# Optimization experiments

Measured on AMD Instinct MI355X. Metric: run time of the kernel, lower is better.

The kernel has to match this reference:

```python
import jax, jax.numpy as jnp
import numpy as np
import math

# AAMsoftmax constants (m=0.2, s=30), matching the torch implementation
M = 0.2
S = 30.0
COS_M = math.cos(M)
SIN_M = math.sin(M)
TH = math.cos(math.pi - M)
MM = math.sin(math.pi - M) * M

B, IN, P, C = 4096, 1024, 256, 5994


def _l2norm(v):
    # F.normalize: v / max(||v||, eps)
    n = jnp.sqrt(jnp.sum(v * v, axis=-1, keepdims=True))
    return v / jnp.maximum(n, 1e-12)


def setup_inputs() -> dict:
    key = jax.random.key(0)
    k0, k1, k2, k3 = jax.random.split(key, 4)
    return {
        "x": jax.random.normal(k0, (B, IN), jnp.float32),
        "label": jax.random.randint(k1, (B,), 0, C, dtype=jnp.int32),
        "W_fc": jax.random.normal(k2, (P, IN), jnp.float32) * (1.0 / np.sqrt(IN)),
        "b_fc": jnp.zeros((P,), jnp.float32),
        "W_aam": jax.random.normal(k3, (C, P), jnp.float32) * 0.05,
    }


def reference(x, label, W_fc, b_fc, W_aam):
    # fc layer: [B, IN] -> [B, P]
    e = x @ W_fc.T + b_fc
    # cosine similarity against class prototypes: [B, C]
    cosine = _l2norm(e) @ _l2norm(W_aam).T
    sine = jnp.sqrt(jnp.clip(1.0 - cosine * cosine, 0.0, 1.0))
    phi = cosine * COS_M - sine * SIN_M
    # easy-margin-off fallback: use cosine - mm where angle too large
    phi = jnp.where((cosine - TH) > 0, phi, cosine - MM)
    one_hot = jax.nn.one_hot(label, C, dtype=cosine.dtype)
    logits = (one_hot * phi + (1.0 - one_hot) * cosine) * S
    # cross-entropy (mean over batch)
    logp = jax.nn.log_softmax(logits, axis=-1)
    nll = -jnp.take_along_axis(logp, label[:, None].astype(jnp.int32), axis=1)[:, 0]
    return jnp.mean(nll)
```

## Files before the change

kernel.cpp:

```cpp
#include <hip/hip_runtime.h>
#include <math.h>

typedef __attribute__((ext_vector_type(8))) short bf16x8;
typedef __attribute__((ext_vector_type(4))) float f32x4;

#define AAM_COS_M 0.9800665778412416f
#define AAM_SIN_M 0.19866933079506122f
#define AAM_TH   (-0.9800665778412416f)
#define AAM_MM    0.03973386615901225f
#define C_CLS 5994

__device__ inline ushort f2bf(float f) {
    unsigned x = __float_as_uint(f);
    return (ushort)((x + 0x7fffu + ((x >> 16) & 1u)) >> 16);
}
__device__ inline float bflo(unsigned u) { return __uint_as_float(u << 16); }
__device__ inline float bfhi(unsigned u) { return __uint_as_float(u & 0xffff0000u); }

__device__ __forceinline__ void gload16(const void* g, void* lds) {
    __builtin_amdgcn_global_load_lds(
        (const __attribute__((address_space(1))) unsigned int*)g,
        (__attribute__((address_space(3))) unsigned int*)lds, 16, 0, 0);
}

__global__ __launch_bounds__(256) void prep(const float* __restrict__ x,
                                            const float* __restrict__ Wfc,
                                            const float* __restrict__ Waam,
                                            ushort* __restrict__ xb,
                                            ushort* __restrict__ wfcb,
                                            ushort* __restrict__ Wn) {
    const int b = blockIdx.x;
    if (b < 4352) {
        const float* s = (b < 4096) ? x : Wfc;
        ushort* d      = (b < 4096) ? xb : wfcb;
        int i = (b < 4096 ? b : b - 4096) * 256 + threadIdx.x;
        float4 v = ((const float4*)s)[i];
        ushort4 o;
        o.x = f2bf(v.x); o.y = f2bf(v.y); o.z = f2bf(v.z); o.w = f2bf(v.w);
        ((ushort4*)d)[i] = o;
    } else {
        const int wave = threadIdx.x >> 6, lane = threadIdx.x & 63;
        const int row = (b - 4352) * 4 + wave;
        ushort4 o;
        if (row < C_CLS) {
            float4 v = ((const float4*)&Waam[(size_t)row * 256])[lane];
            float ss = v.x * v.x + v.y * v.y + v.z * v.z + v.w * v.w;
#pragma unroll
            for (int m = 32; m >= 1; m >>= 1) ss += __shfl_xor(ss, m, 64);
            float sc = 1.f / fmaxf(sqrtf(ss), 1e-12f);
            o.x = f2bf(v.x * sc); o.y = f2bf(v.y * sc);
            o.z = f2bf(v.z * sc); o.w = f2bf(v.w * sc);
        } else {
            o.x = 0; o.y = 0; o.z = 0; o.w = 0;
        }
        ((ushort4*)&Wn[(size_t)row * 256])[lane] = o;
    }
}

__global__ __launch_bounds__(256) void fc_mfma(const ushort* __restrict__ A,
                                               const ushort* __restrict__ Bm,
                                               const float* __restrict__ bias,
                                               float* __restrict__ C) {
    __shared__ ushort As[64 * 32];
    __shared__ ushort Bs[64 * 32];
    const int tid = threadIdx.x, lane = tid & 63, w = tid >> 6;
    const int wr = w >> 1, wc = w & 1;
    const int lx = lane & 15, lg = lane >> 4;
    const int l4 = lane >> 2, c8 = (lane & 3) << 3;
    const int rb = blockIdx.x * 64, cb = blockIdx.y * 64;

    f32x4 zero = {0.f, 0.f, 0.f, 0.f};
    f32x4 acc[2][2];
#pragma unroll
    for (int i = 0; i < 2; ++i)
#pragma unroll
        for (int j = 0; j < 2; ++j) acc[i][j] = zero;

    for (int k0 = 0; k0 < 1024; k0 += 32) {
        gload16(&A[(size_t)(rb + w * 16 + l4) * 1024 + k0 + c8], &As[w * 512]);
        gload16(&Bm[(size_t)(cb + w * 16 + l4) * 1024 + k0 + c8], &Bs[w * 512]);
        __syncthreads();
        bf16x8 af[2], bv[2];
#pragma unroll
        for (int f = 0; f < 2; ++f) {
            af[f] = *(const bf16x8*)&As[(wr * 32 + f * 16 + lx) * 32 + lg * 8];
            bv[f] = *(const bf16x8*)&Bs[(wc * 32 + f * 16 + lx) * 32 + lg * 8];
        }
#pragma unroll
        for (int i = 0; i < 2; ++i)
#pragma unroll
            for (int j = 0; j < 2; ++j)
                acc[i][j] = __builtin_amdgcn_mfma_f32_16x16x32_bf16(af[i], bv[j], acc[i][j], 0, 0, 0);
        __syncthreads();
    }
#pragma unroll
    for (int j = 0; j < 2; ++j) {
        int col = cb + wc * 32 + j * 16 + lx;
        float bb = bias[col];
#pragma unroll
        for (int i = 0; i < 2; ++i) {
            int row0 = rb + wr * 32 + i * 16 + lg * 4;
#pragma unroll
            for (int r = 0; r < 4; ++r)
                C[(size_t)(row0 + r) * 256 + col] = acc[i][j][r] + bb;
        }
    }
}

__global__ __launch_bounds__(256) void rownorm_e(const float* __restrict__ E,
                                                 ushort* __restrict__ En) {
    const int wave = threadIdx.x >> 6, lane = threadIdx.x & 63;
    const int row = blockIdx.x * 4 + wave;
    float4 v = ((const float4*)&E[(size_t)row * 256])[lane];
    float ss = v.x * v.x + v.y * v.y + v.z * v.z + v.w * v.w;
#pragma unroll
    for (int m = 32; m >= 1; m >>= 1) ss += __shfl_xor(ss, m, 64);
    float sc = 1.f / fmaxf(sqrtf(ss), 1e-12f);
    ushort4 o;
    o.x = f2bf(v.x * sc); o.y = f2bf(v.y * sc); o.z = f2bf(v.z * sc); o.w = f2bf(v.w * sc);
    ((ushort4*)&En[(size_t)row * 256])[lane] = o;
}

__global__ __launch_bounds__(256, 2) void aam_mfma(const ushort* __restrict__ A,
                                                   const ushort* __restrict__ Bm,
                                                   const int* __restrict__ lab,
                                                   float* __restrict__ ps,
                                                   float* __restrict__ cosl) {
    __shared__ ushort As[2][128 * 64];
    __shared__ ushort Bs[2][128 * 64];
    const int tid = threadIdx.x, lane = tid & 63, w = tid >> 6;
    const int wr = w >> 1, wc = w & 1;
    const int lx = lane & 15, lg = lane >> 4;
    const int rb = blockIdx.x * 128;
    const int split = blockIdx.y;

    const int lrow = lane >> 3;
    const int gcol = ((lane & 7) ^ lrow) * 8;

    int labs[16];
#pragma unroll
    for (int idx = 0; idx < 16; ++idx)
        labs[idx] = lab[rb + wr * 64 + (idx >> 2) * 16 + lg * 4 + (idx & 3)];

    float srun[16];
#pragma unroll
    for (int idx = 0; idx < 16; ++idx) srun[idx] = 0.f;

    f32x4 zero = {0.f, 0.f, 0.f, 0.f};
    f32x4 acc[4][4];
#pragma unroll
    for (int i = 0; i < 4; ++i)
#pragma unroll
        for (int j = 0; j < 4; ++j) acc[i][j] = zero;

#define AAM_STAGE(buf, g) do {                                                  \
    int t_ = (g) >> 2, k0_ = ((g) & 3) * 64;                                    \
    int cb_ = split * 384 + t_ * 128;                                           \
    _Pragma("unroll")                                                           \
    for (int s_ = 0; s_ < 4; ++s_) {                                            \
        int r0_ = w * 32 + s_ * 8;                                              \
        gload16(&A[(size_t)(rb + r0_ + lrow) * 256 + k0_ + gcol],               \
                &As[buf][r0_ * 64]);                                            \
        gload16(&Bm[(size_t)(cb_ + r0_ + lrow) * 256 + k0_ + gcol],             \
                &Bs[buf][r0_ * 64]);                                            \
    } } while (0)

    int cur = 0;
    AAM_STAGE(0, 0);
    __syncthreads();

    for (int g = 0; g < 12; ++g) {
        if (g < 11) AAM_STAGE(cur ^ 1, g + 1);
#pragma unroll
        for (int kk = 0; kk < 2; ++kk) {
            bf16x8 af[4], bv[4];
#pragma unroll
            for (int f = 0; f < 4; ++f) {
                int ra = wr * 64 + f * 16 + lx;
                int ca = (lg + kk * 4) ^ (lx & 7);
                af[f] = *(const bf16x8*)&As[cur][ra * 64 + ca * 8];
                int rq = wc * 64 + f * 16 + lx;
                bv[f] = *(const bf16x8*)&Bs[cur][rq * 64 + ca * 8];
            }
#pragma unroll
            for (int i = 0; i < 4; ++i)
#pragma unroll
                for (int j = 0; j < 4; ++j)
                    acc[i][j] = __builtin_amdgcn_mfma_f32_16x16x32_bf16(af[i], bv[j], acc[i][j], 0, 0, 0);
        }
        if ((g & 3) == 3) {
            int cb_ = split * 384 + (g >> 2) * 128;
#pragma unroll
            for (int j = 0; j < 4; ++j) {
                int c = cb_ + wc * 64 + j * 16 + lx;
                if (c < C_CLS) {
#pragma unroll
                    for (int i = 0; i < 4; ++i)
#pragma unroll
                        for (int r = 0; r < 4; ++r) {
                            int idx = i * 4 + r;
                            float cosv = acc[i][j][r];
                            srun[idx] += __expf(30.f * cosv - 30.f);
                            if (c == labs[idx])
                                cosl[rb + wr * 64 + i * 16 + lg * 4 + r] = cosv;
                        }
                }
            }
#pragma unroll
            for (int i = 0; i < 4; ++i)
#pragma unroll
                for (int j = 0; j < 4; ++j) acc[i][j] = zero;
        }
        __syncthreads();
        cur ^= 1;
    }
#undef AAM_STAGE

#pragma unroll
    for (int idx = 0; idx < 16; ++idx) {
#pragma unroll
        for (int msk = 1; msk < 16; msk <<= 1)
            srun[idx] += __shfl_xor(srun[idx], msk, 64);
        if (lx == 0) {
            int row = rb + wr * 64 + (idx >> 2) * 16 + lg * 4 + (idx & 3);
            ps[(size_t)row * 32 + split * 2 + wc] = srun[idx];
        }
    }
}

__global__ __launch_bounds__(256) void reduce_nll(const float* __restrict__ ps,
                                                  const float* __restrict__ cosl,
                                                  float* __restrict__ partial) {
    __shared__ float red[4];
    const int row = blockIdx.x * 256 + threadIdx.x;
    const int wave = threadIdx.x >> 6, lane = threadIdx.x & 63;
    float s = 0.f;
#pragma unroll
    for (int q = 0; q < 8; ++q) {
        float4 v = ((const float4*)&ps[(size_t)row * 32])[q];
        s += v.x + v.y + v.z + v.w;
    }
    float cv = cosl[row];
    float sine = sqrtf(fmaxf(1.f - cv * cv, 0.f));
    float phi = cv * AAM_COS_M - sine * AAM_SIN_M;
    phi = ((cv - AAM_TH) > 0.f) ? phi : (cv - AAM_MM);
    float denom = s - __expf(30.f * cv - 30.f) + __expf(30.f * phi - 30.f);
    float nll = 30.f + logf(denom) - 30.f * phi;
#pragma unroll
    for (int m = 32; m >= 1; m >>= 1) nll += __shfl_xor(nll, m, 64);
    if (lane == 0) red[wave] = nll;
    __syncthreads();
    if (threadIdx.x == 0)
        partial[blockIdx.x] = red[0] + red[1] + red[2] + red[3];
}

__global__ __launch_bounds__(64) void final_reduce(const float* __restrict__ partial,
                                                   float* __restrict__ out) {
    const int lane = threadIdx.x;
    float v = (lane < 16) ? partial[lane] : 0.f;
#pragma unroll
    for (int m = 32; m >= 1; m >>= 1) v += __shfl_xor(v, m, 64);
    if (lane == 0) out[0] = v * (1.f / 4096.f);
}

extern "C" void kernel_launch(void* const* d_in, const int* in_sizes, int n_in,
                              void* d_out, int out_size, void* d_ws, size_t ws_size,
                              hipStream_t stream) {
    const float* x    = (const float*)d_in[0];
    const int*   lab  = (const int*)d_in[1];
    const float* Wfc  = (const float*)d_in[2];
    const float* bfc  = (const float*)d_in[3];
    const float* Waam = (const float*)d_in[4];
    float* out = (float*)d_out;

    char* ws = (char*)d_ws;
    ushort* xb   = (ushort*)(ws);
    ushort* Wfcb = (ushort*)(ws + 8388608);
    float*  E    = (float*) (ws + 8912896);
    ushort* En   = (ushort*)(ws);
    ushort* Wn   = (ushort*)(ws + 13107200);
    float*  ps   = (float*) (ws + 16252928);
    float*  cosl = (float*) (ws + 16777216);
    float*  part = (float*) (ws + 16793600);

    prep<<<5888, 256, 0, stream>>>(x, Wfc, Waam, xb, Wfcb, Wn);
    fc_mfma<<<dim3(64, 4), 256, 0, stream>>>(xb, Wfcb, bfc, E);
    rownorm_e<<<1024, 256, 0, stream>>>(E, En);
    aam_mfma<<<dim3(32, 16), 256, 0, stream>>>(En, Wn, lab, ps, cosl);
    reduce_nll<<<16, 256, 0, stream>>>(ps, cosl, part);
    final_reduce<<<1, 64, 0, stream>>>(part, out);
}
```

Before: 120.3 us.

## Fuse fc GEMM with bias and row L2-normalization, convert x to bf16 in-kernel

The separate x-to-bf16 conversion pass and the fp32 E round-trip plus rownorm kernel are removed. A new fc_norm kernel loads fp32 x tiles straight into LDS and converts them to bf16 in registers. Each block computes a full 16x256 output row tile with double-buffered staging, then adds bias, L2-normalizes across waves through shared memory and writes bf16 En directly. This cuts two launches and roughly 16MB of global traffic, but uses only 256 blocks with small per-block M, which may hurt GEMM efficiency and occupancy.

```diff
diff --git a/kernel.cpp b/kernel.cpp
--- a/kernel.cpp
+++ b/kernel.cpp
@@ -14,8 +14,6 @@
     unsigned x = __float_as_uint(f);
     return (ushort)((x + 0x7fffu + ((x >> 16) & 1u)) >> 16);
 }
-__device__ inline float bflo(unsigned u) { return __uint_as_float(u << 16); }
-__device__ inline float bfhi(unsigned u) { return __uint_as_float(u & 0xffff0000u); }
 
 __device__ __forceinline__ void gload16(const void* g, void* lds) {
     __builtin_amdgcn_global_load_lds(
@@ -23,24 +21,20 @@
         (__attribute__((address_space(3))) unsigned int*)lds, 16, 0, 0);
 }
 
-__global__ __launch_bounds__(256) void prep(const float* __restrict__ x,
-                                            const float* __restrict__ Wfc,
+__global__ __launch_bounds__(256) void prep(const float* __restrict__ Wfc,
                                             const float* __restrict__ Waam,
-                                            ushort* __restrict__ xb,
                                             ushort* __restrict__ wfcb,
                                             ushort* __restrict__ Wn) {
     const int b = blockIdx.x;
-    if (b < 4352) {
-        const float* s = (b < 4096) ? x : Wfc;
-        ushort* d      = (b < 4096) ? xb : wfcb;
-        int i = (b < 4096 ? b : b - 4096) * 256 + threadIdx.x;
-        float4 v = ((const float4*)s)[i];
+    if (b < 256) {
+        int i = b * 256 + threadIdx.x;
+        float4 v = ((const float4*)Wfc)[i];
         ushort4 o;
         o.x = f2bf(v.x); o.y = f2bf(v.y); o.z = f2bf(v.z); o.w = f2bf(v.w);
-        ((ushort4*)d)[i] = o;
+        ((ushort4*)wfcb)[i] = o;
     } else {
         const int wave = threadIdx.x >> 6, lane = threadIdx.x & 63;
-        const int row = (b - 4352) * 4 + wave;
+        const int row = (b - 256) * 4 + wave;
         ushort4 o;
         if (row < C_CLS) {
             float4 v = ((const float4*)&Waam[(size_t)row * 256])[lane];
@@ -57,68 +51,95 @@
     }
 }
 
-__global__ __launch_bounds__(256) void fc_mfma(const ushort* __restrict__ A,
+__global__ __launch_bounds__(256) void fc_norm(const float* __restrict__ X,
                                                const ushort* __restrict__ Bm,
                                                const float* __restrict__ bias,
-                                               float* __restrict__ C) {
-    __shared__ ushort As[64 * 32];
-    __shared__ ushort Bs[64 * 32];
+                                               ushort* __restrict__ En) {
+    __shared__ float  Af[2][16 * 32];
+    __shared__ ushort Bs[2][256 * 32];
+    __shared__ float  red[4][16];
     const int tid = threadIdx.x, lane = tid & 63, w = tid >> 6;
-    const int wr = w >> 1, wc = w & 1;
     const int lx = lane & 15, lg = lane >> 4;
-    const int l4 = lane >> 2, c8 = (lane & 3) << 3;
-    const int rb = blockIdx.x * 64, cb = blockIdx.y * 64;
+    const int rb = blockIdx.x * 16;
+
+    const int arow = lane >> 3;
+    const int agcol = ((lane & 7) ^ arow) * 4;
+    const int brow = lane >> 2;
+    const int bgcol = (((lane & 3) ^ (brow & 3)) * 8);
 
     f32x4 zero = {0.f, 0.f, 0.f, 0.f};
-    f32x4 acc[2][2];
-#pragma unroll
-    for (int i = 0; i < 2; ++i)
-#pragma unroll
-        for (int j = 0; j < 2; ++j) acc[i][j] = zero;
-
-    for (int k0 = 0; k0 < 1024; k0 += 32) {
-        gload16(&A[(size_t)(rb + w * 16 + l4) * 1024 + k0 + c8], &As[w * 512]);
-        gload16(&Bm[(size_t)(cb + w * 16 + l4) * 1024 + k0 + c8], &Bs[w * 512]);
+    f32x4 acc[4];
+#pragma unroll
+    for (int j = 0; j < 4; ++j) acc[j] = zero;
+
+#define FC_STAGE(buf, k0) do {                                                  \
+    if (w < 2)                                                                  \
+        gload16(&X[(size_t)(rb + w * 8 + arow) * 1024 + (k0) + agcol],          \
+                &Af[buf][w * 256]);                                             \
+    _Pragma("unroll")                                                           \
+    for (int s_ = 0; s_ < 4; ++s_) {                                            \
+        int r0_ = w * 64 + s_ * 16;                                             \
+        gload16(&Bm[(size_t)(r0_ + brow) * 1024 + (k0) + bgcol],                \
+                &Bs[buf][r0_ * 32]);                                            \
+    } } while (0)
+
+    int cur = 0;
+    FC_STAGE(0, 0);
+    __syncthreads();
+
+    for (int g = 0; g < 32; ++g) {
+        if (g < 31) FC_STAGE(cur ^ 1, (g + 1) * 32);
+        float4 fa0 = *(const float4*)&Af[cur][lx * 32 + (((lg * 2)     ^ (lx & 7)) * 4)];
+        float4 fa1 = *(const float4*)&Af[cur][lx * 32 + (((lg * 2 + 1) ^ (lx & 7)) * 4)];
+        bf16x8 af;
+        af[0] = (short)f2bf(fa0.x); af[1] = (short)f2bf(fa0.y);
+        af[2] = (short)f2bf(fa0.z); af[3] = (short)f2bf(fa0.w);
+        af[4] = (short)f2bf(fa1.x); af[5] = (short)f2bf(fa1.y);
+        af[6] = (short)f2bf(fa1.z); af[7] = (short)f2bf(fa1.w);
+        bf16x8 bv[4];
+#pragma unroll
+        for (int j = 0; j < 4; ++j) {
+            int rq = w * 64 + j * 16 + lx;
+            bv[j] = *(const bf16x8*)&Bs[cur][rq * 32 + ((lg ^ (rq & 3)) * 8)];
+        }
+#pragma unroll
+        for (int j = 0; j < 4; ++j)
+            acc[j] = __builtin_amdgcn_mfma_f32_16x16x32_bf16(af, bv[j], acc[j], 0, 0, 0);
         __syncthreads();
-        bf16x8 af[2], bv[2];
-#pragma unroll
-        for (int f = 0; f < 2; ++f) {
-            af[f] = *(const bf16x8*)&As[(wr * 32 + f * 16 + lx) * 32 + lg * 8];
-            bv[f] = *(const bf16x8*)&Bs[(wc * 32 + f * 16 + lx) * 32 + lg * 8];
-        }
-#pragma unroll
-        for (int i = 0; i < 2; ++i)
-#pragma unroll
-            for (int j = 0; j < 2; ++j)
-                acc[i][j] = __builtin_amdgcn_mfma_f32_16x16x32_bf16(af[i], bv[j], acc[i][j], 0, 0, 0);
-        __syncthreads();
-    }
-#pragma unroll
-    for (int j = 0; j < 2; ++j) {
-        int col = cb + wc * 32 + j * 16 + lx;
-        float bb = bias[col];
-#pragma unroll
-        for (int i = 0; i < 2; ++i) {
-            int row0 = rb + wr * 32 + i * 16 + lg * 4;
-#pragma unroll
-            for (int r = 0; r < 4; ++r)
-                C[(size_t)(row0 + r) * 256 + col] = acc[i][j][r] + bb;
-        }
-    }
-}
-
-__global__ __launch_bounds__(256) void rownorm_e(const float* __restrict__ E,
-                                                 ushort* __restrict__ En) {
-    const int wave = threadIdx.x >> 6, lane = threadIdx.x & 63;
-    const int row = blockIdx.x * 4 + wave;
-    float4 v = ((const float4*)&E[(size_t)row * 256])[lane];
-    float ss = v.x * v.x + v.y * v.y + v.z * v.z + v.w * v.w;
-#pragma unroll
-    for (int m = 32; m >= 1; m >>= 1) ss += __shfl_xor(ss, m, 64);
-    float sc = 1.f / fmaxf(sqrtf(ss), 1e-12f);
-    ushort4 o;
-    o.x = f2bf(v.x * sc); o.y = f2bf(v.y * sc); o.z = f2bf(v.z * sc); o.w = f2bf(v.w * sc);
-    ((ushort4*)&En[(size_t)row * 256])[lane] = o;
+        cur ^= 1;
+    }
+#undef FC_STAGE
+
+    float v[4][4];
+#pragma unroll
+    for (int j = 0; j < 4; ++j) {
+        float bb = bias[w * 64 + j * 16 + lx];
+#pragma unroll
+        for (int q = 0; q < 4; ++q) v[j][q] = acc[j][q] + bb;
+    }
+    float sq[4];
+#pragma unroll
+    for (int q = 0; q < 4; ++q) {
+        float s = v[0][q] * v[0][q] + v[1][q] * v[1][q]
+                + v[2][q] * v[2][q] + v[3][q] * v[3][q];
+#pragma unroll
+        for (int m = 8; m >= 1; m >>= 1) s += __shfl_xor(s, m, 64);
+        sq[q] = s;
+    }
+    if (lx == 0) {
+#pragma unroll
+        for (int q = 0; q < 4; ++q) red[w][lg * 4 + q] = sq[q];
+    }
+    __syncthreads();
+#pragma unroll
+    for (int q = 0; q < 4; ++q) {
+        int row = lg * 4 + q;
+        float tot = red[0][row] + red[1][row] + red[2][row] + red[3][row];
+        float sc = 1.f / fmaxf(sqrtf(tot), 1e-12f);
+#pragma unroll
+        for (int j = 0; j < 4; ++j)
+            En[(size_t)(rb + row) * 256 + w * 64 + j * 16 + lx] = f2bf(v[j][q] * sc);
+    }
 }
 
 __global__ __launch_bounds__(256, 2) void aam_mfma(const ushort* __restrict__ A,
@@ -274,18 +295,15 @@
     float* out = (float*)d_out;
 
     char* ws = (char*)d_ws;
-    ushort* xb   = (ushort*)(ws);
-    ushort* Wfcb = (ushort*)(ws + 8388608);
-    float*  E    = (float*) (ws + 8912896);
     ushort* En   = (ushort*)(ws);
-    ushort* Wn   = (ushort*)(ws + 13107200);
-    float*  ps   = (float*) (ws + 16252928);
-    float*  cosl = (float*) (ws + 16777216);
-    float*  part = (float*) (ws + 16793600);
-
-    prep<<<5888, 256, 0, stream>>>(x, Wfc, Waam, xb, Wfcb, Wn);
-    fc_mfma<<<dim3(64, 4), 256, 0, stream>>>(xb, Wfcb, bfc, E);
-    rownorm_e<<<1024, 256, 0, stream>>>(E, En);
+    ushort* Wfcb = (ushort*)(ws + 2097152);
+    ushort* Wn   = (ushort*)(ws + 2621440);
+    float*  ps   = (float*) (ws + 5767168);
+    float*  cosl = (float*) (ws + 6291456);
+    float*  part = (float*) (ws + 6307840);
+
+    prep<<<1792, 256, 0, stream>>>(Wfc, Waam, Wfcb, Wn);
+    fc_norm<<<256, 256, 0, stream>>>(x, Wfcb, bfc, En);
     aam_mfma<<<dim3(32, 16), 256, 0, stream>>>(En, Wn, lab, ps, cosl);
     reduce_nll<<<16, 256, 0, stream>>>(ps, cosl, part);
     final_reduce<<<1, 64, 0, stream>>>(part, out);
```

After: 128.4 us. 1.07x slower.
